# Kernel tuning notes

Hardware: AMD Instinct MI355X
Metric: run time of the kernel (lower is better)

## Reference

```python
import jax, jax.numpy as jnp
import numpy as np

B, T, D, H, L = 2048, 100, 51, 128, 3  # batch, window, vars, latent, layers


def _lstm_cell(x, h, c, Wih, Whh, b):
    # PyTorch gate order: i, f, g, o. b = b_ih + b_hh (mathematically identical).
    g = x @ Wih.T + h @ Whh.T + b
    i, f, gg, o = jnp.split(g, 4, axis=-1)
    i = jax.nn.sigmoid(i)
    f = jax.nn.sigmoid(f)
    gg = jnp.tanh(gg)
    o = jax.nn.sigmoid(o)
    c_new = f * c + i * gg
    h_new = o * jnp.tanh(c_new)
    return h_new, c_new


def _run_layer(xs, Wih, Whh, b):
    # xs: [T, B, in]; returns full h sequence and final (h, c)
    bsz = xs.shape[1]
    h0 = jnp.zeros((bsz, H), xs.dtype)
    c0 = jnp.zeros((bsz, H), xs.dtype)

    def step(carry, x):
        h, c = carry
        h, c = _lstm_cell(x, h, c, Wih, Whh, b)
        return (h, c), h

    (hT, cT), hs = jax.lax.scan(step, (h0, c0), xs)
    return hs, hT, cT


def setup_inputs() -> dict:
    key = jax.random.key(0)
    ks = iter(jax.random.split(key, 32))
    s = 0.05

    def w(shape):
        return jax.random.normal(next(ks), shape, dtype=jnp.float32) * s

    inp = {"src": jax.random.normal(next(ks), (B, T, D), dtype=jnp.float32)}
    # encoder LSTM params (layer0 input=D, layers1-2 input=H)
    for l in range(L):
        din = D if l == 0 else H
        inp[f"eW{l}"] = w((4 * H, din))
        inp[f"eU{l}"] = w((4 * H, H))
        inp[f"eb{l}"] = w((4 * H,))
    # decoder LSTM params (same input sizes: input_size=input_dim)
    for l in range(L):
        din = D if l == 0 else H
        inp[f"dW{l}"] = w((4 * H, din))
        inp[f"dU{l}"] = w((4 * H, H))
        inp[f"db{l}"] = w((4 * H,))
    inp["fW"] = w((D, H))
    inp["fb"] = w((D,))
    return inp


def reference(src, eW0, eU0, eb0, eW1, eU1, eb1, eW2, eU2, eb2,
              dW0, dU0, db0, dW1, dU1, db1, dW2, dU2, db2, fW, fb):
    bsz, seq, dvar = src.shape
    xs = jnp.transpose(src, (1, 0, 2))  # [T, B, D]

    # ----- encoder: 3 stacked LSTM layers (dropout is identity at eval) -----
    enc = [(eW0, eU0, eb0), (eW1, eU1, eb1), (eW2, eU2, eb2)]
    hs_fin, cs_fin = [], []
    cur = xs
    for (Wih, Whh, b) in enc:
        cur, hT, cT = _run_layer(cur, Wih, Whh, b)
        hs_fin.append(hT)
        cs_fin.append(cT)

    dec = [(dW0, dU0, db0), (dW1, dU1, db1), (dW2, dU2, db2)]
    x0 = jnp.zeros((bsz, dvar), src.dtype)

    def dec_step(carry, _):
        x, (h0, h1, h2), (c0, c1, c2) = carry
        h0, c0 = _lstm_cell(x, h0, c0, *dec[0])
        h1, c1 = _lstm_cell(h0, h1, c1, *dec[1])
        h2, c2 = _lstm_cell(h1, h2, c2, *dec[2])
        pred = h2 @ fW.T + fb  # note: self.relu is defined but never applied
        return (pred, (h0, h1, h2), (c0, c1, c2)), pred

    carry0 = (x0, tuple(hs_fin), tuple(cs_fin))
    _, preds = jax.lax.scan(dec_step, carry0, None, length=seq)  # [T, B, D]

    # cat along time then reverse time axis (inv_idx)
    out = jnp.transpose(preds, (1, 0, 2))[:, ::-1, :]
    return out
```

## Files before the change

kernel.cpp:

```cpp
#include <hip/hip_runtime.h>
#include <stdint.h>

#define Tn 100
#define Dn 51
#define Hn 128
#define G4 512
#define BR 8
#define NWG 256
#define NTH 1024
#define RP 264

typedef unsigned int uint32;
typedef unsigned short u16;
typedef short s16x8 __attribute__((ext_vector_type(8)));
typedef float f32x4v __attribute__((ext_vector_type(4)));

__device__ __forceinline__ float rcp_(float x){ return __builtin_amdgcn_rcpf(x); }
__device__ __forceinline__ float sigm(float x){ return rcp_(1.f + __expf(-x)); }
__device__ __forceinline__ float tanh_(float x){ return 1.f - 2.f*rcp_(1.f + __expf(2.f*x)); }

__device__ __forceinline__ u16 f2bf(float f){
  uint32 u = __float_as_uint(f);
  return (u16)((u + 0x7fffu + ((u >> 16) & 1u)) >> 16);
}
__device__ __forceinline__ float bf2f(u16 u){ return __uint_as_float(((uint32)u)<<16); }

__device__ __forceinline__ void wr_xh(u16* __restrict__ hi, u16* __restrict__ lo,
                                      int idx, float v){
  u16 h = f2bf(v);
  hi[idx] = h;
  lo[idx] = f2bf(v - bf2f(h));
}

struct WP {
  const float* W[6];
  const float* U[6];
  const float* Bb[6];
  const float* fW;
  const float* fb;
};

#define PREP_TOTAL (6*131072 + 6*512 + 8192 + 64)
__global__ void prep_kernel(WP p, u16* __restrict__ wsw, float* __restrict__ bias,
                            float* __restrict__ fwt, float* __restrict__ fbw)
{
  int gid = blockIdx.x*256 + threadIdx.x;
  if (gid >= PREP_TOTAL) return;
  if (gid < 6*131072){
    int l = gid >> 17;
    int e = gid & 131071;
    int n    = e >> 12;
    int s    = (e >> 9) & 7;
    int lane = (e >> 3) & 63;
    int j    = e & 7;
    int k = s*32 + (lane >> 4)*8 + j;
    int c = n*16 + (lane & 15);
    int din = (l % 3 == 0) ? Dn : Hn;
    int K = din + Hn;
    u16 v = 0;
    if (k < K){
      float f = (k < din) ? p.W[l][(size_t)c*din + k] : p.U[l][(size_t)c*Hn + (k - din)];
      v = f2bf(f);
    }
    wsw[gid] = v;
  } else if (gid < 6*131072 + 6*512){
    int i = gid - 6*131072;
    bias[i] = p.Bb[i>>9][i & 511];
  } else if (gid < 6*131072 + 6*512 + 8192){
    int i = gid - (6*131072 + 6*512);
    int k = i >> 6, d = i & 63;
    fwt[i] = (d < Dn) ? p.fW[(size_t)d*Hn + k] : 0.f;
  } else {
    int d = gid - (6*131072 + 6*512 + 8192);
    fbw[d] = (d < Dn) ? p.fb[d] : 0.f;
  }
}

template<int S>
__device__ __forceinline__ void gemm_mfma(const u16* __restrict__ wsl,
                                          const float* __restrict__ bl,
                                          const u16* __restrict__ xh_hi,
                                          const u16* __restrict__ xh_lo,
                                          float* __restrict__ gates, int tid)
{
  const int wave = tid >> 6, lane = tid & 63;
  const int mrow = lane & 15, kgrp = lane >> 4;
  const int n0 = wave*2;
  const u16* bp0 = wsl + n0*4096 + lane*8;
  const u16* bp1 = bp0 + 4096;
  const int aoff = mrow*RP + kgrp*8;
  f32x4v acc0 = {0.f,0.f,0.f,0.f}, acc1 = {0.f,0.f,0.f,0.f};
  #pragma unroll 2
  for (int s=0; s<S; s++){
    s16x8 b0 = *(const s16x8*)(bp0 + s*512);
    s16x8 b1 = *(const s16x8*)(bp1 + s*512);
    s16x8 ah = *(const s16x8*)(xh_hi + aoff + s*32);
    s16x8 al = *(const s16x8*)(xh_lo + aoff + s*32);
    acc0 = __builtin_amdgcn_mfma_f32_16x16x32_bf16(ah, b0, acc0, 0, 0, 0);
    acc1 = __builtin_amdgcn_mfma_f32_16x16x32_bf16(ah, b1, acc1, 0, 0, 0);
    acc0 = __builtin_amdgcn_mfma_f32_16x16x32_bf16(al, b0, acc0, 0, 0, 0);
    acc1 = __builtin_amdgcn_mfma_f32_16x16x32_bf16(al, b1, acc1, 0, 0, 0);
  }
  if (kgrp < 2){
    int rb = kgrp*4;
    int c0g = n0*16 + mrow, c1g = c0g + 16;
    float bv0 = bl[c0g], bv1 = bl[c1g];
    #pragma unroll
    for (int v=0; v<4; v++){
      gates[(rb+v)*G4 + c0g] = acc0[v] + bv0;
      gates[(rb+v)*G4 + c1g] = acc1[v] + bv1;
    }
  }
}

__device__ __forceinline__ void activate(const float* __restrict__ gates,
                                         float* __restrict__ h, float* __restrict__ c, int tid)
{
  int r = tid >> 7, j = tid & 127;
  const float* g = gates + r*G4;
  float ig = sigm (g[j]);
  float fg = sigm (g[j + Hn]);
  float gg = tanh_(g[j + 2*Hn]);
  float og = sigm (g[j + 3*Hn]);
  int hi = r*Hn + j;
  float cn = fg*c[hi] + ig*gg;
  c[hi] = cn;
  h[hi] = og*tanh_(cn);
}

__device__ __forceinline__ void build_src(u16* __restrict__ hi, u16* __restrict__ lo,
                                          const float* __restrict__ src,
                                          long b0, int t, const float* __restrict__ h0, int tid)
{
  int k = tid & 255;
  #pragma unroll
  for (int it=0; it<2; it++){
    int r = (tid >> 8) + it*4;
    if (k < 192){
      float v;
      if (k < Dn) v = src[((size_t)(b0+r)*Tn + t)*Dn + k];
      else if (k < Dn + Hn) v = h0[r*Hn + (k - Dn)];
      else v = 0.f;
      wr_xh(hi, lo, r*RP + k, v);
    }
  }
}

__device__ __forceinline__ void build_pred(u16* __restrict__ hi, u16* __restrict__ lo,
                                           const float* __restrict__ pred,
                                           const float* __restrict__ h0, int tid)
{
  int k = tid & 255;
  #pragma unroll
  for (int it=0; it<2; it++){
    int r = (tid >> 8) + it*4;
    if (k < 192){
      float v;
      if (k < Dn) v = pred[r*64 + k];
      else if (k < Dn + Hn) v = h0[r*Hn + (k - Dn)];
      else v = 0.f;
      wr_xh(hi, lo, r*RP + k, v);
    }
  }
}

__device__ __forceinline__ void build_mid(u16* __restrict__ hi, u16* __restrict__ lo,
                                          const float* __restrict__ hlow,
                                          const float* __restrict__ hl, int tid)
{
  int k = tid & 255;
  #pragma unroll
  for (int it=0; it<2; it++){
    int r = (tid >> 8) + it*4;
    float v = (k < Hn) ? hlow[r*Hn + k] : hl[r*Hn + (k - Hn)];
    wr_xh(hi, lo, r*RP + k, v);
  }
}

__device__ __forceinline__ void proj_out(const float* __restrict__ h2, const float* __restrict__ fwt,
                                         const float* __restrict__ fbw, float* __restrict__ pred,
                                         float* __restrict__ out, long b0, int t, int tid)
{
  if (tid < 512){
    int r = tid >> 6, d = tid & 63;
    const float* h = h2 + r*Hn;
    float acc = 0.f;
    #pragma unroll 8
    for (int k=0;k<Hn;k++) acc += h[k] * fwt[k*64 + d];
    if (d < Dn){
      float pv = acc + fbw[d];
      pred[r*64 + d] = pv;
      out[((size_t)(b0+r)*Tn + (Tn-1-t))*Dn + d] = pv;
    }
  }
}

__global__ __launch_bounds__(NTH, 4) void lstm_kernel(
    const float* __restrict__ src, const u16* __restrict__ wsw,
    const float* __restrict__ bias, const float* __restrict__ fwt,
    const float* __restrict__ fbw, float* __restrict__ out)
{
  __shared__ __align__(16) u16   xh_hi[16*RP];
  __shared__ __align__(16) u16   xh_lo[16*RP];
  __shared__ __align__(16) float gates[BR*G4];
  __shared__ __align__(16) float hS[3*BR*Hn];
  __shared__ __align__(16) float cS[3*BR*Hn];
  __shared__ __align__(16) float pred[BR*64];

  const int tid = threadIdx.x;
  const long b0 = (long)blockIdx.x * BR;

  for (int i=tid; i<16*RP; i+=NTH){ xh_hi[i]=0; xh_lo[i]=0; }
  for (int i=tid; i<3*BR*Hn; i+=NTH){ hS[i]=0.f; cS[i]=0.f; }
  __syncthreads();

  for (int t=0;t<Tn;t++){
    build_src(xh_hi, xh_lo, src, b0, t, hS, tid);
    __syncthreads();
    gemm_mfma<6>(wsw + 0*131072, bias + 0*G4, xh_hi, xh_lo, gates, tid);
    __syncthreads();
    activate(gates, hS, cS, tid);
    __syncthreads();

    build_mid(xh_hi, xh_lo, hS, hS + BR*Hn, tid);
    __syncthreads();
    gemm_mfma<8>(wsw + 1*131072, bias + 1*G4, xh_hi, xh_lo, gates, tid);
    __syncthreads();
    activate(gates, hS + BR*Hn, cS + BR*Hn, tid);
    __syncthreads();

    build_mid(xh_hi, xh_lo, hS + BR*Hn, hS + 2*BR*Hn, tid);
    __syncthreads();
    gemm_mfma<8>(wsw + 2*131072, bias + 2*G4, xh_hi, xh_lo, gates, tid);
    __syncthreads();
    activate(gates, hS + 2*BR*Hn, cS + 2*BR*Hn, tid);
    __syncthreads();
  }

  if (tid < 512) pred[tid] = 0.f;
  __syncthreads();

  for (int t=0;t<Tn;t++){
    build_pred(xh_hi, xh_lo, pred, hS, tid);
    __syncthreads();
    gemm_mfma<6>(wsw + 3*131072, bias + 3*G4, xh_hi, xh_lo, gates, tid);
    __syncthreads();
    activate(gates, hS, cS, tid);
    __syncthreads();

    build_mid(xh_hi, xh_lo, hS, hS + BR*Hn, tid);
    __syncthreads();
    gemm_mfma<8>(wsw + 4*131072, bias + 4*G4, xh_hi, xh_lo, gates, tid);
    __syncthreads();
    activate(gates, hS + BR*Hn, cS + BR*Hn, tid);
    __syncthreads();

    build_mid(xh_hi, xh_lo, hS + BR*Hn, hS + 2*BR*Hn, tid);
    __syncthreads();
    gemm_mfma<8>(wsw + 5*131072, bias + 5*G4, xh_hi, xh_lo, gates, tid);
    __syncthreads();
    activate(gates, hS + 2*BR*Hn, cS + 2*BR*Hn, tid);
    __syncthreads();

    proj_out(hS + 2*BR*Hn, fwt, fbw, pred, out, b0, t, tid);
    __syncthreads();
  }
}

extern "C" void kernel_launch(void* const* d_in, const int* in_sizes, int n_in,
                              void* d_out, int out_size, void* d_ws, size_t ws_size,
                              hipStream_t stream)
{
  (void)in_sizes; (void)n_in; (void)out_size; (void)ws_size;
  const float* src = (const float*)d_in[0];
  WP p;
  for (int l=0;l<3;l++){
    p.W[l]    = (const float*)d_in[1  + 3*l];
    p.U[l]    = (const float*)d_in[2  + 3*l];
    p.Bb[l]   = (const float*)d_in[3  + 3*l];
    p.W[3+l]  = (const float*)d_in[10 + 3*l];
    p.U[3+l]  = (const float*)d_in[11 + 3*l];
    p.Bb[3+l] = (const float*)d_in[12 + 3*l];
  }
  p.fW = (const float*)d_in[19];
  p.fb = (const float*)d_in[20];

  u16*   wsw  = (u16*)d_ws;
  float* bias = (float*)((char*)d_ws + 6*131072*sizeof(u16));
  float* fwt  = bias + 6*512;
  float* fbw  = fwt + 8192;

  prep_kernel<<<(PREP_TOTAL + 255)/256, 256, 0, stream>>>(p, wsw, bias, fwt, fbw);
  lstm_kernel<<<NWG, NTH, 0, stream>>>(src, wsw, bias, fwt, fbw, (float*)d_out);
}
```

Baseline: 2.063 ms.

## Stack hi/lo bf16 split rows into one MFMA A tile, halving MFMA count

The hi and lo bf16 parts of the activation are now stored as rows 0-7 and 8-15 of a single 16-row A tile. The old code padded the 8 real batch rows to 16 and issued separate MFMAs for hi and lo. Each K step now issues two MFMAs instead of four, and the hi and lo partial sums are combined with a cross-lane shuffle (shfl_down by 32) before bias and store. The K loop is also fully unrolled. This halves the matrix-core work per gate GEMM, at the cost of an extra shuffle reduction and more registers from the full unroll.

```diff
diff --git a/kernel.cpp b/kernel.cpp
--- a/kernel.cpp
+++ b/kernel.cpp
@@ -25,11 +25,10 @@
 }
 __device__ __forceinline__ float bf2f(u16 u){ return __uint_as_float(((uint32)u)<<16); }
 
-__device__ __forceinline__ void wr_xh(u16* __restrict__ hi, u16* __restrict__ lo,
-                                      int idx, float v){
+__device__ __forceinline__ void wr_xh(u16* __restrict__ xhA, int r, int k, float v){
   u16 h = f2bf(v);
-  hi[idx] = h;
-  lo[idx] = f2bf(v - bf2f(h));
+  xhA[r*RP + k]     = h;
+  xhA[(r+8)*RP + k] = f2bf(v - bf2f(h));
 }
 
 struct WP {
@@ -79,27 +78,29 @@
 template<int S>
 __device__ __forceinline__ void gemm_mfma(const u16* __restrict__ wsl,
                                           const float* __restrict__ bl,
-                                          const u16* __restrict__ xh_hi,
-                                          const u16* __restrict__ xh_lo,
+                                          const u16* __restrict__ xhA,
                                           float* __restrict__ gates, int tid)
 {
   const int wave = tid >> 6, lane = tid & 63;
   const int mrow = lane & 15, kgrp = lane >> 4;
   const int n0 = wave*2;
   const u16* bp0 = wsl + n0*4096 + lane*8;
-  const u16* bp1 = bp0 + 4096;
   const int aoff = mrow*RP + kgrp*8;
   f32x4v acc0 = {0.f,0.f,0.f,0.f}, acc1 = {0.f,0.f,0.f,0.f};
-  #pragma unroll 2
+  #pragma unroll
   for (int s=0; s<S; s++){
+    s16x8 a  = *(const s16x8*)(xhA + aoff + s*32);
     s16x8 b0 = *(const s16x8*)(bp0 + s*512);
-    s16x8 b1 = *(const s16x8*)(bp1 + s*512);
-    s16x8 ah = *(const s16x8*)(xh_hi + aoff + s*32);
-    s16x8 al = *(const s16x8*)(xh_lo + aoff + s*32);
-    acc0 = __builtin_amdgcn_mfma_f32_16x16x32_bf16(ah, b0, acc0, 0, 0, 0);
-    acc1 = __builtin_amdgcn_mfma_f32_16x16x32_bf16(ah, b1, acc1, 0, 0, 0);
-    acc0 = __builtin_amdgcn_mfma_f32_16x16x32_bf16(al, b0, acc0, 0, 0, 0);
-    acc1 = __builtin_amdgcn_mfma_f32_16x16x32_bf16(al, b1, acc1, 0, 0, 0);
+    s16x8 b1 = *(const s16x8*)(bp0 + 4096 + s*512);
+    acc0 = __builtin_amdgcn_mfma_f32_16x16x32_bf16(a, b0, acc0, 0, 0, 0);
+    acc1 = __builtin_amdgcn_mfma_f32_16x16x32_bf16(a, b1, acc1, 0, 0, 0);
+  }
+  #pragma unroll
+  for (int v=0; v<4; v++){
+    float l0 = __shfl_down(acc0[v], 32);
+    float l1 = __shfl_down(acc1[v], 32);
+    acc0[v] += l0;
+    acc1[v] += l1;
   }
   if (kgrp < 2){
     int rb = kgrp*4;
@@ -128,7 +129,7 @@
   h[hi] = og*tanh_(cn);
 }
 
-__device__ __forceinline__ void build_src(u16* __restrict__ hi, u16* __restrict__ lo,
+__device__ __forceinline__ void build_src(u16* __restrict__ xhA,
                                           const float* __restrict__ src,
                                           long b0, int t, const float* __restrict__ h0, int tid)
 {
@@ -141,12 +142,12 @@
       if (k < Dn) v = src[((size_t)(b0+r)*Tn + t)*Dn + k];
       else if (k < Dn + Hn) v = h0[r*Hn + (k - Dn)];
       else v = 0.f;
-      wr_xh(hi, lo, r*RP + k, v);
-    }
-  }
-}
-
-__device__ __forceinline__ void build_pred(u16* __restrict__ hi, u16* __restrict__ lo,
+      wr_xh(xhA, r, k, v);
+    }
+  }
+}
+
+__device__ __forceinline__ void build_pred(u16* __restrict__ xhA,
                                            const float* __restrict__ pred,
                                            const float* __restrict__ h0, int tid)
 {
@@ -159,12 +160,12 @@
       if (k < Dn) v = pred[r*64 + k];
       else if (k < Dn + Hn) v = h0[r*Hn + (k - Dn)];
       else v = 0.f;
-      wr_xh(hi, lo, r*RP + k, v);
-    }
-  }
-}
-
-__device__ __forceinline__ void build_mid(u16* __restrict__ hi, u16* __restrict__ lo,
+      wr_xh(xhA, r, k, v);
+    }
+  }
+}
+
+__device__ __forceinline__ void build_mid(u16* __restrict__ xhA,
                                           const float* __restrict__ hlow,
                                           const float* __restrict__ hl, int tid)
 {
@@ -173,7 +174,7 @@
   for (int it=0; it<2; it++){
     int r = (tid >> 8) + it*4;
     float v = (k < Hn) ? hlow[r*Hn + k] : hl[r*Hn + (k - Hn)];
-    wr_xh(hi, lo, r*RP + k, v);
+    wr_xh(xhA, r, k, v);
   }
 }
 
@@ -200,8 +201,7 @@
     const float* __restrict__ bias, const float* __restrict__ fwt,
     const float* __restrict__ fbw, float* __restrict__ out)
 {
-  __shared__ __align__(16) u16   xh_hi[16*RP];
-  __shared__ __align__(16) u16   xh_lo[16*RP];
+  __shared__ __align__(16) u16   xhA[16*RP];
   __shared__ __align__(16) float gates[BR*G4];
   __shared__ __align__(16) float hS[3*BR*Hn];
   __shared__ __align__(16) float cS[3*BR*Hn];
@@ -210,28 +210,28 @@
   const int tid = threadIdx.x;
   const long b0 = (long)blockIdx.x * BR;
 
-  for (int i=tid; i<16*RP; i+=NTH){ xh_hi[i]=0; xh_lo[i]=0; }
+  for (int i=tid; i<16*RP; i+=NTH) xhA[i]=0;
   for (int i=tid; i<3*BR*Hn; i+=NTH){ hS[i]=0.f; cS[i]=0.f; }
   __syncthreads();
 
   for (int t=0;t<Tn;t++){
-    build_src(xh_hi, xh_lo, src, b0, t, hS, tid);
-    __syncthreads();
-    gemm_mfma<6>(wsw + 0*131072, bias + 0*G4, xh_hi, xh_lo, gates, tid);
+    build_src(xhA, src, b0, t, hS, tid);
+    __syncthreads();
+    gemm_mfma<6>(wsw + 0*131072, bias + 0*G4, xhA, gates, tid);
     __syncthreads();
     activate(gates, hS, cS, tid);
     __syncthreads();
 
-    build_mid(xh_hi, xh_lo, hS, hS + BR*Hn, tid);
-    __syncthreads();
-    gemm_mfma<8>(wsw + 1*131072, bias + 1*G4, xh_hi, xh_lo, gates, tid);
+    build_mid(xhA, hS, hS + BR*Hn, tid);
+    __syncthreads();
+    gemm_mfma<8>(wsw + 1*131072, bias + 1*G4, xhA, gates, tid);
     __syncthreads();
     activate(gates, hS + BR*Hn, cS + BR*Hn, tid);
     __syncthreads();
 
-    build_mid(xh_hi, xh_lo, hS + BR*Hn, hS + 2*BR*Hn, tid);
-    __syncthreads();
-    gemm_mfma<8>(wsw + 2*131072, bias + 2*G4, xh_hi, xh_lo, gates, tid);
+    build_mid(xhA, hS + BR*Hn, hS + 2*BR*Hn, tid);
+    __syncthreads();
+    gemm_mfma<8>(wsw + 2*131072, bias + 2*G4, xhA, gates, tid);
     __syncthreads();
     activate(gates, hS + 2*BR*Hn, cS + 2*BR*Hn, tid);
     __syncthreads();
@@ -241,23 +241,23 @@
   __syncthreads();
 
   for (int t=0;t<Tn;t++){
-    build_pred(xh_hi, xh_lo, pred, hS, tid);
-    __syncthreads();
-    gemm_mfma<6>(wsw + 3*131072, bias + 3*G4, xh_hi, xh_lo, gates, tid);
+    build_pred(xhA, pred, hS, tid);
+    __syncthreads();
+    gemm_mfma<6>(wsw + 3*131072, bias + 3*G4, xhA, gates, tid);
     __syncthreads();
     activate(gates, hS, cS, tid);
     __syncthreads();
 
-    build_mid(xh_hi, xh_lo, hS, hS + BR*Hn, tid);
-    __syncthreads();
-    gemm_mfma<8>(wsw + 4*131072, bias + 4*G4, xh_hi, xh_lo, gates, tid);
+    build_mid(xhA, hS, hS + BR*Hn, tid);
+    __syncthreads();
+    gemm_mfma<8>(wsw + 4*131072, bias + 4*G4, xhA, gates, tid);
     __syncthreads();
     activate(gates, hS + BR*Hn, cS + BR*Hn, tid);
     __syncthreads();
 
-    build_mid(xh_hi, xh_lo, hS + BR*Hn, hS + 2*BR*Hn, tid);
-    __syncthreads();
-    gemm_mfma<8>(wsw + 5*131072, bias + 5*G4, xh_hi, xh_lo, gates, tid);
+    build_mid(xhA, hS + BR*Hn, hS + 2*BR*Hn, tid);
+    __syncthreads();
+    gemm_mfma<8>(wsw + 5*131072, bias + 5*G4, xhA, gates, tid);
     __syncthreads();
     activate(gates, hS + 2*BR*Hn, cS + 2*BR*Hn, tid);
     __syncthreads();
```

New measurement: 6.574 ms. 219% more time.
